# Optimization experiments

Hardware: AMD Instinct MI355X
Metric: run time of the kernel (lower is better)

Reference implementation:

```python
import jax, jax.numpy as jnp
import numpy as np

NUM_USERS = 30000
NUM_ITEMS = 30000
N = NUM_USERS + NUM_ITEMS          # total graph nodes (users + items)
E = 800000                          # number of edges
EMBED_K = 64
INTENTS = 4
D = EMBED_K // INTENTS              # per-intent channel chunk
N_LAYERS = 1
ROUTING_ITERS = 2


def setup_inputs() -> dict:
    key = jax.random.key(0)
    k1, k2, k3, k4 = jax.random.split(key, 4)
    Gu = jax.random.normal(k1, (NUM_USERS, EMBED_K), jnp.float32) * 0.1
    Gi = jax.random.normal(k2, (NUM_ITEMS, EMBED_K), jnp.float32) * 0.1
    # head list: guarantee every node appears at least once as a head so that
    # D = 1/sqrt(row_degree) is finite (real CF graphs have no isolated rows)
    edge_h = jnp.concatenate([jnp.arange(N, dtype=jnp.int64),
                              jax.random.randint(k3, (E - N,), 0, N, dtype=jnp.int64)])
    edge_t = jax.random.randint(k4, (E,), 0, N, dtype=jnp.int64)
    return {"Gu": Gu, "Gi": Gi, "edge_h": edge_h, "edge_t": edge_t}


def _l2norm(x, eps=1e-12):
    # matches torch.nn.functional.normalize(dim=-1)
    return x / jnp.sqrt(jnp.maximum(jnp.sum(x * x, axis=-1, keepdims=True), eps))


def reference(Gu, Gi, edge_h, edge_t):
    ego = jnp.concatenate([Gu, Gi], axis=0)            # [N, K]
    all_emb = [ego]
    # routing attention logits per intent per edge (initialized to ones)
    A_values = jnp.ones((INTENTS, E), dtype=Gu.dtype)
    for _ in range(N_LAYERS):
        # split embed dim into INTENTS contiguous chunks -> [I, N, D]
        X = ego.reshape(N, INTENTS, D).transpose(1, 0, 2)
        Z = X
        for _t in range(ROUTING_ITERS):
            # softmax over intents per edge (pick=False path; p_train is always False)
            scores = jax.nn.softmax(A_values, axis=0)                    # [I, E]
            # per-intent row degrees (sparse.sum over dim=1 indexes rows = heads)
            deg = jnp.zeros((INTENTS, N), scores.dtype).at[:, edge_h].add(scores)
            d_col = 1.0 / jnp.sqrt(deg)                                  # [I, N]
            # D_col @ X, A @ (.), D_col @ (.)  -- note original applies D_col twice (as written)
            Y = d_col[..., None] * X                                     # [I, N, D]
            msg = scores[..., None] * Y[:, edge_t, :]                    # [I, E, D]
            Z = jnp.zeros((INTENTS, N, D), X.dtype).at[:, edge_h, :].add(msg)
            Z = d_col[..., None] * Z                                     # [I, N, D]
            # attention update: normalize(head) . tanh(normalize(tail))
            head = _l2norm(Z[:, edge_h, :])                              # [I, E, D]
            tail = _l2norm(X[:, edge_t, :])                              # [I, E, D]
            A_values = A_values + jnp.sum(head * jnp.tanh(tail), axis=-1)
        # concat intent chunks back along channel dim
        ego = Z.transpose(1, 0, 2).reshape(N, EMBED_K)
        all_emb.append(ego)
    out = jnp.mean(jnp.stack(all_emb, axis=1), axis=1)   # [N, K]
    return out[:NUM_USERS], out[NUM_USERS:]
```

## Files before the change

kernel.cpp:

```cpp
#include <hip/hip_runtime.h>
#include <hip/hip_fp16.h>


#define NUSERS 30000
#define NN     60000
#define NNP    (NN + 1)
#define EE     800000
#define SCAN_B ((NN + 255) / 256)
#define EV_B   ((EE / 4 + 255) / 256)
#define NW1_B  ((NN + 1 + 3) / 4)
#define GPI    ((NN + 31) / 32)
#define PIN_B  ((((GPI + 1) / 2) * 8))

__device__ __forceinline__ float getX(const float* __restrict__ Gu,
                                      const float* __restrict__ Gi,
                                      int n, int c) {
    return (n < NUSERS) ? Gu[n * 64 + c] : Gi[(n - NUSERS) * 64 + c];
}

__device__ __forceinline__ int clampN(int n) {
    return ((unsigned)n < (unsigned)NN) ? n : 0;
}

__device__ __forceinline__ __half2 bch2(float f) {
    return __builtin_bit_cast(__half2, f);
}


__global__ void edge_count(const int* __restrict__ eh, int* __restrict__ deg0,
                           int* __restrict__ rank) {
    int e4 = (blockIdx.x * blockDim.x + threadIdx.x) * 4;
    if (e4 >= EE) return;
    int4 h = *(const int4*)(eh + e4);
    int4 r;
    r.x = atomicAdd(&deg0[clampN(h.x)], 1);
    r.y = atomicAdd(&deg0[clampN(h.y)], 1);
    r.z = atomicAdd(&deg0[clampN(h.z)], 1);
    r.w = atomicAdd(&deg0[clampN(h.w)], 1);
    *(int4*)(rank + e4) = r;
}

__global__ void scan_local(const int* __restrict__ deg0, int* __restrict__ offsets,
                           int* __restrict__ bsum, float* __restrict__ d0a) {
    int gid = blockIdx.x * 256 + threadIdx.x;
    int lane = threadIdx.x & 63, w = threadIdx.x >> 6;
    int vdeg = (gid < NN) ? deg0[gid] : 0;
    if (gid < NN) d0a[gid] = rsqrtf(fmaxf(0.25f * (float)vdeg, 1e-30f));
    if (gid == NN) d0a[NN] = 0.f;
    int x = vdeg;
    #pragma unroll
    for (int d = 1; d < 64; d <<= 1) {
        int y = __shfl_up(x, d, 64);
        if (lane >= d) x += y;
    }
    __shared__ int wsum[4];
    if (lane == 63) wsum[w] = x;
    __syncthreads();
    int wpre = 0;
    #pragma unroll
    for (int j = 0; j < 4; ++j) wpre += (j < w) ? wsum[j] : 0;
    int incl = x + wpre;
    if (gid < NN) offsets[gid] = incl - vdeg;
    if (threadIdx.x == 255) bsum[blockIdx.x] = incl;
}

__global__ void scanadd2_prep(int* __restrict__ offsets, const int* __restrict__ bsum,
                              const float* __restrict__ d0a,
                              const float* __restrict__ Gu, const float* __restrict__ Gi,
                              __half* __restrict__ Yq, __half* __restrict__ Tq) {
    if (blockIdx.x < SCAN_B) {
        int tid = threadIdx.x, lane = tid & 63, w = tid >> 6;
        int vv = (tid < SCAN_B) ? bsum[tid] : 0;
        int x = vv;
        #pragma unroll
        for (int d = 1; d < 64; d <<= 1) {
            int y = __shfl_up(x, d, 64);
            if (lane >= d) x += y;
        }
        __shared__ int wsum[4];
        __shared__ int bpre;
        if (lane == 63) wsum[w] = x;
        __syncthreads();
        int wpre = 0;
        #pragma unroll
        for (int j = 0; j < 4; ++j) wpre += (j < w) ? wsum[j] : 0;
        if (tid == blockIdx.x) bpre = x + wpre - vv;
        __syncthreads();
        int gid = blockIdx.x * 256 + tid;
        if (gid < NN) offsets[gid] += bpre;
        if (gid == 0) offsets[NN] = EE;
    } else {
        int n = (blockIdx.x - SCAN_B) * 4 + (threadIdx.x >> 6);
        if (n > NN) return;
        int lane = threadIdx.x & 63;
        int i = lane >> 4, cl = lane & 15;
        float x = (n < NN) ? getX(Gu, Gi, n, lane) : 0.f;
        float sx = x * x;
        #pragma unroll
        for (int m = 1; m < 16; m <<= 1) sx += __shfl_xor(sx, m, 64);
        float invx = rsqrtf(fmaxf(sx, 1e-12f));
        float d0v = d0a[n];
        size_t a = ((size_t)i * NNP + n) * 16 + cl;
        Yq[a] = __float2half(d0v * x);
        Tq[a] = __float2half(tanhf(x * invx));
    }
}

__global__ void scatter(const int* __restrict__ eh, const int* __restrict__ et,
                        const int* __restrict__ rank, const int* __restrict__ offsets,
                        int* __restrict__ csr_tail) {
    int e4 = (blockIdx.x * 256 + threadIdx.x) * 4;
    if (e4 >= EE) return;
    int4 h = *(const int4*)(eh + e4);
    int4 t = *(const int4*)(et + e4);
    int4 r = *(const int4*)(rank + e4);
    int s0 = offsets[clampN(h.x)] + r.x;
    if ((unsigned)s0 < EE) csr_tail[s0] = clampN(t.x);
    int s1 = offsets[clampN(h.y)] + r.y;
    if ((unsigned)s1 < EE) csr_tail[s1] = clampN(t.y);
    int s2 = offsets[clampN(h.z)] + r.z;
    if ((unsigned)s2 < EE) csr_tail[s2] = clampN(t.z);
    int s3 = offsets[clampN(h.w)] + r.w;
    if ((unsigned)s3 < EE) csr_tail[s3] = clampN(t.w);
}

__global__ void zat(const int* __restrict__ offsets, const int* __restrict__ csr_tail,
                    const __half* __restrict__ Yq, const __half* __restrict__ Tq,
                    float* __restrict__ dotq) {
    __shared__ __half zn[32][24];
    __shared__ int soff[33];
    int b = blockIdx.x, tid = threadIdx.x;
    int xcd = b & 7;
    int i = xcd >> 1;
    int g = (b >> 3) * 2 + (xcd & 1);
    if (g >= GPI) return;
    int n0 = g * 32;
    if (tid < 33) soff[tid] = offsets[n0 + tid];
    __syncthreads();

    {
        int g8 = tid >> 3, cl = tid & 7;
        int s0 = soff[g8], s1 = soff[g8 + 1];
        const __half* Yi = Yq + (size_t)i * NNP * 16;
        float accx = 0.f, accy = 0.f;
        for (int base = s0; base < s1; base += 4) {
            #pragma unroll
            for (int u = 0; u < 4; ++u) {
                int kk = base + u;
                bool act = kk < s1;
                int kc = act ? kk : s0;
                int t = act ? csr_tail[kc] : NN;
                __half2 y = *(const __half2*)(Yi + (size_t)t * 16 + cl * 2);
                float2 yf = __half22float2(y);
                accx += yf.x; accy += yf.y;
            }
        }
        float ss = accx * accx + accy * accy;
        ss += __shfl_xor(ss, 1, 64);
        ss += __shfl_xor(ss, 2, 64);
        ss += __shfl_xor(ss, 4, 64);
        float inv = rsqrtf(fmaxf(ss, 1e-12f));
        *(__half2*)&zn[g8][cl * 2] = __floats2half2_rn(accx * inv, accy * inv);
    }
    __syncthreads();

    int e0 = soff[0], e1 = soff[32];
    const __half* Ti = Tq + (size_t)i * NNP * 16;
    for (int k = e0 + tid; k < e1; k += 256) {
        int hl = 0;
        #pragma unroll
        for (int step = 16; step >= 1; step >>= 1)
            if (soff[hl + step] <= k) hl += step;
        int t = csr_tail[k];
        float4 ta = *(const float4*)(Ti + (size_t)t * 16);
        float4 tb = *(const float4*)(Ti + (size_t)t * 16 + 8);
        float4 za = *(const float4*)&zn[hl][0];
        float4 zb = *(const float4*)&zn[hl][8];
        __half2 acc = __floats2half2_rn(0.f, 0.f);
        acc = __hfma2(bch2(za.x), bch2(ta.x), acc);
        acc = __hfma2(bch2(za.y), bch2(ta.y), acc);
        acc = __hfma2(bch2(za.z), bch2(ta.z), acc);
        acc = __hfma2(bch2(za.w), bch2(ta.w), acc);
        acc = __hfma2(bch2(zb.x), bch2(tb.x), acc);
        acc = __hfma2(bch2(zb.y), bch2(tb.y), acc);
        acc = __hfma2(bch2(zb.z), bch2(tb.z), acc);
        acc = __hfma2(bch2(zb.w), bch2(tb.w), acc);
        float2 f = __half22float2(acc);
        dotq[(size_t)i * EE + k] = f.x + f.y;
    }
}

__global__ void combine(const int* __restrict__ offsets, const float* __restrict__ dotq,
                        const float* __restrict__ d0a,
                        __half* __restrict__ sq, float* __restrict__ d1q,
                        float* __restrict__ d1rd0q) {
    int n = blockIdx.x * 4 + (threadIdx.x >> 6);
    if (n >= NN) return;
    int lane = threadIdx.x & 63;
    int s0 = offsets[n], s1 = offsets[n + 1];
    float sum0 = 0.f, sum1 = 0.f, sum2 = 0.f, sum3 = 0.f;
    for (int k = s0 + lane; k < s1; k += 64) {
        float v0 = dotq[k];
        float v1 = dotq[EE + k];
        float v2 = dotq[2 * EE + k];
        float v3 = dotq[3 * EE + k];
        float mx = fmaxf(fmaxf(v0, v1), fmaxf(v2, v3));
        float e0 = __expf(v0 - mx), e1 = __expf(v1 - mx);
        float e2 = __expf(v2 - mx), e3 = __expf(v3 - mx);
        float inv = 1.f / (e0 + e1 + e2 + e3);
        e0 *= inv; e1 *= inv; e2 *= inv; e3 *= inv;
        sq[k]          = __float2half(e0);
        sq[EE + k]     = __float2half(e1);
        sq[2 * EE + k] = __float2half(e2);
        sq[3 * EE + k] = __float2half(e3);
        sum0 += e0; sum1 += e1; sum2 += e2; sum3 += e3;
    }
    #pragma unroll
    for (int m = 1; m < 64; m <<= 1) {
        sum0 += __shfl_xor(sum0, m, 64);
        sum1 += __shfl_xor(sum1, m, 64);
        sum2 += __shfl_xor(sum2, m, 64);
        sum3 += __shfl_xor(sum3, m, 64);
    }
    if (lane < 4) {
        float ds = (lane == 0) ? sum0 : (lane == 1) ? sum1 : (lane == 2) ? sum2 : sum3;
        float d1 = rsqrtf(fmaxf(ds, 1e-30f));
        d1q[(size_t)lane * NNP + n] = d1;
        d1rd0q[(size_t)lane * NNP + n] = d1 / d0a[n];
    }
}

__global__ void outk(const int* __restrict__ offsets, const int* __restrict__ csr_tail,
                     const __half* __restrict__ Yq, const __half* __restrict__ sq,
                     const float* __restrict__ d1q, const float* __restrict__ d1rd0q,
                     const float* __restrict__ Gu, const float* __restrict__ Gi,
                     float* __restrict__ out) {
    int b = blockIdx.x, tid = threadIdx.x;
    int xcd = b & 7;
    int i = xcd >> 1;
    int g = (b >> 3) * 2 + (xcd & 1);
    if (g >= GPI) return;
    int n = g * 32 + (tid >> 3);
    int cl = tid & 7;
    int s0 = offsets[n], s1 = offsets[n + 1];
    const __half* Yi = Yq + (size_t)i * NNP * 16;
    const __half* si = sq + (size_t)i * EE;
    const float* w1 = d1rd0q + (size_t)i * NNP;
    float accx = 0.f, accy = 0.f;
    for (int base = s0; base < s1; base += 4) {
        #pragma unroll
        for (int u = 0; u < 4; ++u) {
            int kk = base + u;
            bool act = kk < s1;
            int kc = act ? kk : s0;
            int t = csr_tail[kc];
            float s = act ? __half2float(si[kc]) : 0.f;
            float w = s * w1[t];
            __half2 y = *(const __half2*)(Yi + (size_t)t * 16 + cl * 2);
            float2 yf = __half22float2(y);
            accx = fmaf(w, yf.x, accx);
            accy = fmaf(w, yf.y, accy);
        }
    }
    float d = d1q[(size_t)i * NNP + n];
    int ch = i * 16 + cl * 2;
    const float* xr = (n < NUSERS) ? (Gu + (size_t)n * 64 + ch)
                                   : (Gi + (size_t)(n - NUSERS) * 64 + ch);
    float2 x2 = *(const float2*)xr;
    float2 o;
    o.x = 0.5f * (x2.x + d * accx);
    o.y = 0.5f * (x2.y + d * accy);
    *(float2*)(out + (size_t)n * 64 + ch) = o;
}


extern "C" void kernel_launch(void* const* d_in, const int* in_sizes, int n_in,
                              void* d_out, int out_size, void* d_ws, size_t ws_size,
                              hipStream_t stream) {
    const float* Gu = (const float*)d_in[0];
    const float* Gi = (const float*)d_in[1];
    const int* eh = (const int*)d_in[2];
    const int* et = (const int*)d_in[3];
    float* out = (float*)d_out;

    char* p = (char*)d_ws;
    float*  dotq     = (float*)p;      p += (size_t)EE * 4 * 4;
    __half* sq       = (__half*)p;     p += (size_t)EE * 4 * 2;
    int*    csr_tail = (int*)p;        p += (size_t)EE * 4;
    int*    rank     = (int*)p;        p += (size_t)EE * 4;
    int*    offsets  = (int*)p;        p += ((size_t)NNP * 4 + 15) / 16 * 16;
    int*    deg0     = (int*)p;        p += (size_t)NN * 4;
    int*    bsum     = (int*)p;        p += ((size_t)SCAN_B * 4 + 15) / 16 * 16;
    float*  d0a      = (float*)p;      p += ((size_t)NNP * 4 + 15) / 16 * 16;
    float*  d1q      = (float*)p;      p += (size_t)4 * NNP * 4;
    float*  d1rd0q   = (float*)p;      p += (size_t)4 * NNP * 4;
    __half* Yq       = (__half*)p;     p += (size_t)4 * NNP * 16 * 2;
    __half* Tq       = (__half*)p;

    hipMemsetAsync(deg0, 0, NN * sizeof(int), stream);
    edge_count<<<EV_B, 256, 0, stream>>>(eh, deg0, rank);
    scan_local<<<SCAN_B, 256, 0, stream>>>(deg0, offsets, bsum, d0a);
    scanadd2_prep<<<SCAN_B + NW1_B, 256, 0, stream>>>(offsets, bsum, d0a,
                                                      Gu, Gi, Yq, Tq);
    scatter<<<EV_B, 256, 0, stream>>>(eh, et, rank, offsets, csr_tail);

    zat<<<PIN_B, 256, 0, stream>>>(offsets, csr_tail, Yq, Tq, dotq);

    combine<<<(NN + 3) / 4, 256, 0, stream>>>(offsets, dotq, d0a, sq, d1q, d1rd0q);

    outk<<<PIN_B, 256, 0, stream>>>(offsets, csr_tail, Yq, sq, d1q, d1rd0q,
                                    Gu, Gi, out);
}
```

Measured before the change: 258.2 us.

## Store logits in fp16, interleave scores per edge, restructure final aggregation node-major

Attention logits are now written as half precision, which halves that intermediate traffic. Softmax scores are stored interleaved per edge as four halves, so one 8-byte load serves all intents. The final aggregation kernel now processes one node per 32 lanes covering all 64 channels, gathering a new fp16 copy of the raw embedding with the d1 factor indexed per node and intent. This replaces the per-intent gathers and the d1/d0 ratio array. In exchange it writes an extra fp16 embedding copy and accepts reduced precision in the logits.

```diff
diff --git a/kernel.cpp b/kernel.cpp
--- a/kernel.cpp
+++ b/kernel.cpp
@@ -9,6 +9,8 @@
 #define SCAN_B ((NN + 255) / 256)
 #define EV_B   ((EE / 4 + 255) / 256)
 #define NW1_B  ((NN + 1 + 3) / 4)
+#define NW_B   ((NN + 3) / 4)
+#define N8_B   (NN / 8)
 #define GPI    ((NN + 31) / 32)
 #define PIN_B  ((((GPI + 1) / 2) * 8))
 
@@ -67,7 +69,8 @@
 __global__ void scanadd2_prep(int* __restrict__ offsets, const int* __restrict__ bsum,
                               const float* __restrict__ d0a,
                               const float* __restrict__ Gu, const float* __restrict__ Gi,
-                              __half* __restrict__ Yq, __half* __restrict__ Tq) {
+                              __half* __restrict__ Yq, __half* __restrict__ Tq,
+                              __half* __restrict__ Xh) {
     if (blockIdx.x < SCAN_B) {
         int tid = threadIdx.x, lane = tid & 63, w = tid >> 6;
         int vv = (tid < SCAN_B) ? bsum[tid] : 0;
@@ -103,6 +106,7 @@
         size_t a = ((size_t)i * NNP + n) * 16 + cl;
         Yq[a] = __float2half(d0v * x);
         Tq[a] = __float2half(tanhf(x * invx));
+        Xh[(size_t)n * 64 + lane] = __float2half(x);
     }
 }
 
@@ -126,7 +130,7 @@
 
 __global__ void zat(const int* __restrict__ offsets, const int* __restrict__ csr_tail,
                     const __half* __restrict__ Yq, const __half* __restrict__ Tq,
-                    float* __restrict__ dotq) {
+                    __half* __restrict__ dotq) {
     __shared__ __half zn[32][24];
     __shared__ int soff[33];
     int b = blockIdx.x, tid = threadIdx.x;
@@ -186,33 +190,33 @@
         acc = __hfma2(bch2(zb.z), bch2(tb.z), acc);
         acc = __hfma2(bch2(zb.w), bch2(tb.w), acc);
         float2 f = __half22float2(acc);
-        dotq[(size_t)i * EE + k] = f.x + f.y;
-    }
-}
-
-__global__ void combine(const int* __restrict__ offsets, const float* __restrict__ dotq,
-                        const float* __restrict__ d0a,
-                        __half* __restrict__ sq, float* __restrict__ d1q,
-                        float* __restrict__ d1rd0q) {
+        dotq[(size_t)i * EE + k] = __float2half(f.x + f.y);
+    }
+}
+
+__global__ void combine(const int* __restrict__ offsets, const __half* __restrict__ dotq,
+                        __half* __restrict__ s4, float* __restrict__ dcol1) {
     int n = blockIdx.x * 4 + (threadIdx.x >> 6);
     if (n >= NN) return;
     int lane = threadIdx.x & 63;
     int s0 = offsets[n], s1 = offsets[n + 1];
     float sum0 = 0.f, sum1 = 0.f, sum2 = 0.f, sum3 = 0.f;
     for (int k = s0 + lane; k < s1; k += 64) {
-        float v0 = dotq[k];
-        float v1 = dotq[EE + k];
-        float v2 = dotq[2 * EE + k];
-        float v3 = dotq[3 * EE + k];
+        float v0 = __half2float(dotq[k]);
+        float v1 = __half2float(dotq[EE + k]);
+        float v2 = __half2float(dotq[2 * EE + k]);
+        float v3 = __half2float(dotq[3 * EE + k]);
         float mx = fmaxf(fmaxf(v0, v1), fmaxf(v2, v3));
         float e0 = __expf(v0 - mx), e1 = __expf(v1 - mx);
         float e2 = __expf(v2 - mx), e3 = __expf(v3 - mx);
         float inv = 1.f / (e0 + e1 + e2 + e3);
         e0 *= inv; e1 *= inv; e2 *= inv; e3 *= inv;
-        sq[k]          = __float2half(e0);
-        sq[EE + k]     = __float2half(e1);
-        sq[2 * EE + k] = __float2half(e2);
-        sq[3 * EE + k] = __float2half(e3);
+        __half2 q01 = __floats2half2_rn(e0, e1);
+        __half2 q23 = __floats2half2_rn(e2, e3);
+        int2 st;
+        st.x = __builtin_bit_cast(int, q01);
+        st.y = __builtin_bit_cast(int, q23);
+        *(int2*)(s4 + (size_t)k * 4) = st;
         sum0 += e0; sum1 += e1; sum2 += e2; sum3 += e3;
     }
     #pragma unroll
@@ -224,28 +228,21 @@
     }
     if (lane < 4) {
         float ds = (lane == 0) ? sum0 : (lane == 1) ? sum1 : (lane == 2) ? sum2 : sum3;
-        float d1 = rsqrtf(fmaxf(ds, 1e-30f));
-        d1q[(size_t)lane * NNP + n] = d1;
-        d1rd0q[(size_t)lane * NNP + n] = d1 / d0a[n];
+        dcol1[n * 4 + lane] = rsqrtf(fmaxf(ds, 1e-30f));
     }
 }
 
 __global__ void outk(const int* __restrict__ offsets, const int* __restrict__ csr_tail,
-                     const __half* __restrict__ Yq, const __half* __restrict__ sq,
-                     const float* __restrict__ d1q, const float* __restrict__ d1rd0q,
+                     const __half* __restrict__ Xh, const __half* __restrict__ s4,
+                     const float* __restrict__ dcol1,
                      const float* __restrict__ Gu, const float* __restrict__ Gi,
                      float* __restrict__ out) {
-    int b = blockIdx.x, tid = threadIdx.x;
-    int xcd = b & 7;
-    int i = xcd >> 1;
-    int g = (b >> 3) * 2 + (xcd & 1);
-    if (g >= GPI) return;
-    int n = g * 32 + (tid >> 3);
-    int cl = tid & 7;
+    int tid = threadIdx.x;
+    int n = blockIdx.x * 8 + (tid >> 5);
+    if (n >= NN) return;
+    int cc = tid & 31;
+    int i = cc >> 3;
     int s0 = offsets[n], s1 = offsets[n + 1];
-    const __half* Yi = Yq + (size_t)i * NNP * 16;
-    const __half* si = sq + (size_t)i * EE;
-    const float* w1 = d1rd0q + (size_t)i * NNP;
     float accx = 0.f, accy = 0.f;
     for (int base = s0; base < s1; base += 4) {
         #pragma unroll
@@ -254,16 +251,19 @@
             bool act = kk < s1;
             int kc = act ? kk : s0;
             int t = csr_tail[kc];
-            float s = act ? __half2float(si[kc]) : 0.f;
-            float w = s * w1[t];
-            __half2 y = *(const __half2*)(Yi + (size_t)t * 16 + cl * 2);
+            int2 raw = *(const int2*)(s4 + (size_t)kc * 4);
+            int word = (cc & 16) ? raw.y : raw.x;
+            unsigned short us = (unsigned short)(word >> ((cc & 8) ? 16 : 0));
+            float s = act ? __half2float(__builtin_bit_cast(__half, us)) : 0.f;
+            float w = s * dcol1[t * 4 + i];
+            __half2 y = *(const __half2*)(Xh + (size_t)t * 64 + cc * 2);
             float2 yf = __half22float2(y);
             accx = fmaf(w, yf.x, accx);
             accy = fmaf(w, yf.y, accy);
         }
     }
-    float d = d1q[(size_t)i * NNP + n];
-    int ch = i * 16 + cl * 2;
+    float d = dcol1[n * 4 + i];
+    int ch = cc * 2;
     const float* xr = (n < NUSERS) ? (Gu + (size_t)n * 64 + ch)
                                    : (Gi + (size_t)(n - NUSERS) * 64 + ch);
     float2 x2 = *(const float2*)xr;
@@ -284,30 +284,29 @@
     float* out = (float*)d_out;
 
     char* p = (char*)d_ws;
-    float*  dotq     = (float*)p;      p += (size_t)EE * 4 * 4;
-    __half* sq       = (__half*)p;     p += (size_t)EE * 4 * 2;
+    __half* dotq     = (__half*)p;     p += (size_t)EE * 4 * 2;
+    __half* s4       = (__half*)p;     p += (size_t)EE * 4 * 2;
     int*    csr_tail = (int*)p;        p += (size_t)EE * 4;
     int*    rank     = (int*)p;        p += (size_t)EE * 4;
     int*    offsets  = (int*)p;        p += ((size_t)NNP * 4 + 15) / 16 * 16;
     int*    deg0     = (int*)p;        p += (size_t)NN * 4;
     int*    bsum     = (int*)p;        p += ((size_t)SCAN_B * 4 + 15) / 16 * 16;
     float*  d0a      = (float*)p;      p += ((size_t)NNP * 4 + 15) / 16 * 16;
-    float*  d1q      = (float*)p;      p += (size_t)4 * NNP * 4;
-    float*  d1rd0q   = (float*)p;      p += (size_t)4 * NNP * 4;
+    float*  dcol1    = (float*)p;      p += (size_t)NN * 4 * 4;
     __half* Yq       = (__half*)p;     p += (size_t)4 * NNP * 16 * 2;
-    __half* Tq       = (__half*)p;
+    __half* Tq       = (__half*)p;     p += (size_t)4 * NNP * 16 * 2;
+    __half* Xh       = (__half*)p;
 
     hipMemsetAsync(deg0, 0, NN * sizeof(int), stream);
     edge_count<<<EV_B, 256, 0, stream>>>(eh, deg0, rank);
     scan_local<<<SCAN_B, 256, 0, stream>>>(deg0, offsets, bsum, d0a);
     scanadd2_prep<<<SCAN_B + NW1_B, 256, 0, stream>>>(offsets, bsum, d0a,
-                                                      Gu, Gi, Yq, Tq);
+                                                      Gu, Gi, Yq, Tq, Xh);
     scatter<<<EV_B, 256, 0, stream>>>(eh, et, rank, offsets, csr_tail);
 
     zat<<<PIN_B, 256, 0, stream>>>(offsets, csr_tail, Yq, Tq, dotq);
 
-    combine<<<(NN + 3) / 4, 256, 0, stream>>>(offsets, dotq, d0a, sq, d1q, d1rd0q);
-
-    outk<<<PIN_B, 256, 0, stream>>>(offsets, csr_tail, Yq, sq, d1q, d1rd0q,
-                                    Gu, Gi, out);
-}
+    combine<<<NW_B, 256, 0, stream>>>(offsets, dotq, s4, dcol1);
+
+    outk<<<N8_B, 256, 0, stream>>>(offsets, csr_tail, Xh, s4, dcol1, Gu, Gi, out);
+}
```

Measured after the change: 245.6 us. 1.05x faster.
